# Kernel tuning notes

Measured on AMD Instinct MI355X. Metric: run time of the kernel, lower is better.

The kernel has to match this reference:

```python
import jax, jax.numpy as jnp
import numpy as np

K = 1.0      # Lorentz curvature param (geoopt convention: <x,x>_L = -K)
SQK = 1.0    # sqrt(K)
B, LOOKBACK, SEG, D = 256, 4096, 32, 256
N = LOOKBACK // SEG  # 128 segments


def _mink_inner(x, y):
    # Minkowski inner product, keepdims on last axis
    return -x[..., :1] * y[..., :1] + jnp.sum(x[..., 1:] * y[..., 1:], axis=-1, keepdims=True)


def _expmap0_spatial(v):
    # v: [..., D] spatial tangent at origin -> point on hyperboloid [..., D+1]
    n = jnp.linalg.norm(v, axis=-1, keepdims=True)
    ns = jnp.maximum(n, 1e-9)
    x0 = SQK * jnp.cosh(n / SQK)
    xr = SQK * jnp.sinh(n / SQK) * v / ns
    return jnp.concatenate([x0, xr], axis=-1)


def _projx(x):
    # re-project onto hyperboloid: x0 = sqrt(K + ||x_spatial||^2)
    xr = x[..., 1:]
    x0 = jnp.sqrt(K + jnp.sum(xr * xr, axis=-1, keepdims=True))
    return jnp.concatenate([x0, xr], axis=-1)


def _origin_like(x):
    return jnp.zeros_like(x).at[..., 0].set(SQK)


def _logmap(x, y):
    # log_x(y) on the Lorentz manifold
    alpha = jnp.maximum(-_mink_inner(x, y) / K, 1.0 + 1e-7)
    dist = SQK * jnp.arccosh(alpha)
    u = y - alpha * x  # tangent direction (unnormalized)
    un = jnp.sqrt(jnp.maximum(_mink_inner(u, u), 1e-12))
    return dist * u / un


def _expmap(x, u):
    # exp_x(u) on the Lorentz manifold
    un = jnp.sqrt(jnp.maximum(_mink_inner(u, u), 1e-12))
    theta = un / SQK
    return jnp.cosh(theta) * x + jnp.sinh(theta) * SQK * u / un


def _clip_norm(v, max_norm):
    # euclidean-norm clip (torch.norm semantics in source)
    n = jnp.linalg.norm(v, axis=-1, keepdims=True)
    return v / jnp.maximum(n, 1e-12) * jnp.minimum(n, max_norm)


def _encode(x, W, b):
    # [B, lookback] -> [B, N, D]; dropout is identity at eval
    xs = x.reshape(B, N, SEG)
    return jnp.einsum('bns,ds->bnd', xs, W) + b


def _to_hyperbolic(z, effective_scale):
    # vectorized over all segments (original looped over seg_idx)
    v = z * jnp.tanh(effective_scale)
    n = jnp.maximum(jnp.linalg.norm(v, axis=-1, keepdims=True), 1e-8)
    v = v / n * jnp.minimum(n, 1.5)
    return _projx(_expmap0_spatial(v))


def _lorentz_fusion(pts, w):
    # pts: [4, B, N, D+1], w: [4] softmax weights; weighted Karcher mean
    o = _origin_like(pts[0])
    t0 = _logmap(o, pts)                       # tangents at origin (time comp == 0)
    wt = _clip_norm(jnp.einsum('c,cbnd->bnd', w, t0), 2.0)
    mean = _projx(_expmap0_spatial(wt[..., 1:]))  # geoopt expmap0 uses spatial part
    for _ in range(5):                         # fixed 5 Karcher iterations
        tv = _logmap(mean, pts)                # [4, B, N, D+1]
        wv = _clip_norm(jnp.einsum('c,cbnd->bnd', w, tv), 2.0)
        mean = _projx(_expmap(mean, 0.1 * wv))
    return mean


def setup_inputs() -> dict:
    key = jax.random.key(0)
    ks = jax.random.split(key, 12)
    wscale = 1.0 / np.sqrt(SEG)
    inp = {
        'trend': jax.random.normal(ks[0], (B, LOOKBACK), jnp.float32),
        'seasonal_coarse': jax.random.normal(ks[1], (B, LOOKBACK), jnp.float32),
        'seasonal_fine': jax.random.normal(ks[2], (B, LOOKBACK), jnp.float32),
        'residual': jax.random.normal(ks[3], (B, LOOKBACK), jnp.float32),
        'W_trend': jax.random.normal(ks[4], (D, SEG), jnp.float32) * wscale,
        'b_trend': jnp.zeros((D,), jnp.float32),
        'W_coarse': jax.random.normal(ks[5], (D, SEG), jnp.float32) * wscale,
        'b_coarse': jnp.zeros((D,), jnp.float32),
        'W_fine': jax.random.normal(ks[6], (D, SEG), jnp.float32) * wscale,
        'b_fine': jnp.zeros((D,), jnp.float32),
        'W_residual': jax.random.normal(ks[7], (D, SEG), jnp.float32) * wscale,
        'b_residual': jnp.zeros((D,), jnp.float32),
        'effective_scale': jnp.asarray(0.001, jnp.float32),
        'lorentz_weights': jnp.ones((4,), jnp.float32) * 0.25,
    }
    return inp


def reference(trend, seasonal_coarse, seasonal_fine, residual,
              W_trend, b_trend, W_coarse, b_coarse, W_fine, b_fine,
              W_residual, b_residual, effective_scale, lorentz_weights):
    z_t = _encode(trend, W_trend, b_trend)
    z_c = _encode(seasonal_coarse, W_coarse, b_coarse)
    z_f = _encode(seasonal_fine, W_fine, b_fine)
    z_r = _encode(residual, W_residual, b_residual)
    h_t = _to_hyperbolic(z_t, effective_scale)
    h_c = _to_hyperbolic(z_c, effective_scale)
    h_f = _to_hyperbolic(z_f, effective_scale)
    h_r = _to_hyperbolic(z_r, effective_scale)
    w = jax.nn.softmax(lorentz_weights)
    combined = _lorentz_fusion(jnp.stack([h_t, h_c, h_f, h_r], axis=0), w)
    return (h_t, h_c, h_f, h_r, combined)
```

## Files before the change

kernel.cpp:

```cpp
#include <hip/hip_runtime.h>
#include <math.h>

namespace {

typedef float f4 __attribute__((ext_vector_type(4)));

constexpr int PPW  = 4;
constexpr int WPB  = 4;
constexpr int PPB  = PPW * WPB;
constexpr int NPTS = 256 * 128;
constexpr int GRID = NPTS / PPB;
constexpr int OUTS = 257;
constexpr size_t HOFF = (size_t)NPTS * OUTS;
constexpr int WSTR = 256;
constexpr int HSTR = 260;

__device__ __forceinline__ float frcp(float x)   { return __builtin_amdgcn_rcpf(x); }
__device__ __forceinline__ float fsqrt_(float x) { return __builtin_amdgcn_sqrtf(x); }
__device__ __forceinline__ float facosh(float a) {
  return __logf(a + fsqrt_(fmaf(a, a, -1.f)));
}
__device__ __forceinline__ void fsinhcosh(float x, float& sh, float& ch) {
  float e = __expf(x), ei = frcp(e);
  sh = 0.5f * (e - ei);
  ch = 0.5f * (e + ei);
}
__device__ __forceinline__ float fsinh(float x) {
  float e = __expf(x);
  return 0.5f * (e - frcp(e));
}
__device__ __forceinline__ float dot4(f4 a, f4 b) {
  return a.x * b.x + a.y * b.y + a.z * b.z + a.w * b.w;
}
__device__ __forceinline__ f4 fma4s(float a, f4 b, f4 c) {
  f4 av = {a, a, a, a};
  return __builtin_elementwise_fma(av, b, c);
}

template <int CTRL>
__device__ __forceinline__ float dpp_add(float x) {
  int t = __builtin_amdgcn_update_dpp(0, __builtin_bit_cast(int, x), CTRL, 0xf, 0xf, true);
  return x + __builtin_bit_cast(float, t);
}

template <int NB>
__device__ __forceinline__ void grp_reduce(float* v) {
#pragma unroll
  for (int i = 0; i < NB; ++i) {
    float t = v[i];
    t = dpp_add<0x128>(t);
    t = dpp_add<0x124>(t);
    t = dpp_add<0x122>(t);
    t = dpp_add<0x121>(t);
    v[i] = t;
  }
}

__global__ __launch_bounds__(256) void splmw_kernel(
    const float* __restrict__ xt, const float* __restrict__ xc,
    const float* __restrict__ xf, const float* __restrict__ xr,
    const float* __restrict__ Wt, const float* __restrict__ bt,
    const float* __restrict__ Wc, const float* __restrict__ bc,
    const float* __restrict__ Wf, const float* __restrict__ bf,
    const float* __restrict__ Wr, const float* __restrict__ br,
    const float* __restrict__ esp, const float* __restrict__ lwp,
    float* __restrict__ out) {
  __shared__ float wlds[32 * WSTR];
  __shared__ float hlds[WPB * PPW * HSTR];

  const int tid  = threadIdx.x;
  const int lane = tid & 63;
  const int m    = lane & 15;
  const int grp  = lane >> 4;
  const int wv   = __builtin_amdgcn_readfirstlane(tid >> 6);
  const int pt0  = blockIdx.x * PPB + wv * PPW;
  const int pt   = pt0 + grp;
  float* hw = hlds + wv * (PPW * HSTR);

  float es2 = __expf(2.f * esp[0]);
  const float ts = (es2 - 1.f) * frcp(es2 + 1.f);
  float l0 = lwp[0], l1 = lwp[1], l2 = lwp[2], l3 = lwp[3];
  float mx = fmaxf(fmaxf(l0, l1), fmaxf(l2, l3));
  float e0 = __expf(l0 - mx), e1 = __expf(l1 - mx);
  float e2 = __expf(l2 - mx), e3 = __expf(l3 - mx);
  float ei = frcp(e0 + e1 + e2 + e3);
  const float wgt[4] = {e0 * ei, e1 * ei, e2 * ei, e3 * ei};

  const float* xsarr[4] = {xt, xc, xf, xr};
  const float* Wsarr[4] = {Wt, Wc, Wf, Wr};
  const float* Bsarr[4] = {bt, bc, bf, br};

  f4    h[4][4];
  float x0s[4];
  float r2s[4];

#pragma unroll
  for (int c = 0; c < 4; ++c) {
    const float* Wp = Wsarr[c];
    f4 wrow[8];
#pragma unroll
    for (int k = 0; k < 8; ++k) wrow[k] = *(const f4*)(Wp + tid * 32 + 4 * k);
    __syncthreads();
#pragma unroll
    for (int k = 0; k < 8; ++k) {
      wlds[(4 * k + 0) * WSTR + tid] = wrow[k].x;
      wlds[(4 * k + 1) * WSTR + tid] = wrow[k].y;
      wlds[(4 * k + 2) * WSTR + tid] = wrow[k].z;
      wlds[(4 * k + 3) * WSTR + tid] = wrow[k].w;
    }
    __syncthreads();

    f4 acc[PPW];
    {
      f4 bv = ((const f4*)Bsarr[c])[lane];
#pragma unroll
      for (int p = 0; p < PPW; ++p) acc[p] = bv;
    }
    const float* xp = xsarr[c] + (size_t)pt0 * 32;
#pragma unroll
    for (int s4 = 0; s4 < 8; ++s4) {
      f4 q0 = *(const f4*)(xp + 4 * s4);
      f4 q1 = *(const f4*)(xp + 32 + 4 * s4);
      f4 q2 = *(const f4*)(xp + 64 + 4 * s4);
      f4 q3 = *(const f4*)(xp + 96 + 4 * s4);
      float qa[4][4] = {{q0.x, q0.y, q0.z, q0.w}, {q1.x, q1.y, q1.z, q1.w},
                        {q2.x, q2.y, q2.z, q2.w}, {q3.x, q3.y, q3.z, q3.w}};
#pragma unroll
      for (int si = 0; si < 4; ++si) {
        f4 w4 = *(const f4*)&wlds[(4 * s4 + si) * WSTR + 4 * lane];
#pragma unroll
        for (int p = 0; p < PPW; ++p) acc[p] = fma4s(qa[p][si], w4, acc[p]);
      }
    }

#pragma unroll
    for (int p = 0; p < PPW; ++p) *(f4*)&hw[p * HSTR + 4 * lane] = acc[p];
    __builtin_amdgcn_wave_barrier();
    f4 zj[4];
#pragma unroll
    for (int j = 0; j < 4; ++j) zj[j] = *(const f4*)&hw[grp * HSTR + 4 * m + 64 * j];

    float pa = 0.f;
#pragma unroll
    for (int j = 0; j < 4; ++j) {
      h[c][j] = ts * zj[j];
      pa += dot4(h[c][j], h[c][j]);
    }
    grp_reduce<1>(&pa);
    {
      float n1  = fsqrt_(pa);
      float n1m = fmaxf(n1, 1e-8f);
      float c1  = fminf(n1m, 1.5f) * frcp(n1m);
      float n2  = c1 * n1;
      float nsx = fmaxf(n2, 1e-9f);
      float sh  = fsinh(n2);
      float rn  = frcp(nsx);
      float g   = sh * c1 * rn;
      float sxr = sh * n2 * rn;
      float xx0 = fsqrt_(fmaf(sxr, sxr, 1.f));
#pragma unroll
      for (int j = 0; j < 4; ++j) h[c][j] = g * h[c][j];
      x0s[c] = xx0;
      r2s[c] = g * g * pa;
      float* o = out + (size_t)c * HOFF + (size_t)pt * OUTS;
      if (m == 0) o[0] = xx0;
#pragma unroll
      for (int j = 0; j < 4; ++j) {
        int base = 1 + 4 * m + 64 * j;
        f4 v = h[c][j];
        o[base] = v.x; o[base + 1] = v.y; o[base + 2] = v.z; o[base + 3] = v.w;
      }
    }
  }

  float wt0 = 0.f;
  f4    wtr[4];
#pragma unroll
  for (int j = 0; j < 4; ++j) wtr[j] = (f4){0.f, 0.f, 0.f, 0.f};
#pragma unroll
  for (int c = 0; c < 4; ++c) {
    float y0    = x0s[c];
    float alpha = fmaxf(y0, 1.f + 1e-7f);
    float dist  = facosh(alpha);
    float u0    = y0 - alpha;
    float msq   = r2s[c] - u0 * u0;
    float un    = fsqrt_(fmaxf(msq, 1e-12f));
    float f     = wgt[c] * dist * frcp(un);
    wt0 = fmaf(f, u0, wt0);
#pragma unroll
    for (int j = 0; j < 4; ++j) wtr[j] = fma4s(f, h[c][j], wtr[j]);
  }
  float rrp = 0.f;
#pragma unroll
  for (int j = 0; j < 4; ++j) rrp += dot4(wtr[j], wtr[j]);
  grp_reduce<1>(&rrp);

  f4    mr[4];
  float mrr, m0;
  {
    float rr  = rrp;
    float nrm = fsqrt_(fmaf(wt0, wt0, rr));
    float scl = fminf(nrm, 2.f) * frcp(fmaxf(nrm, 1e-12f));
    float nr  = scl * fsqrt_(rr);
    float nsx = fmaxf(nr, 1e-9f);
    float g   = fsinh(nr) * scl * frcp(nsx);
#pragma unroll
    for (int j = 0; j < 4; ++j) mr[j] = g * wtr[j];
    mrr = g * g * rr;
    m0  = fsqrt_(1.f + mrr);
  }

#pragma unroll 1
  for (int it = 0; it < 5; ++it) {
    float dots[4];
#pragma unroll
    for (int c = 0; c < 4; ++c) {
      float d = 0.f;
#pragma unroll
      for (int j = 0; j < 4; ++j) d += dot4(mr[j], h[c][j]);
      dots[c] = d;
    }
    grp_reduce<4>(dots);

    float wv0 = 0.f;
    f4    wvr[4];
#pragma unroll
    for (int j = 0; j < 4; ++j) wvr[j] = (f4){0.f, 0.f, 0.f, 0.f};
#pragma unroll
    for (int c = 0; c < 4; ++c) {
      float d     = dots[c];
      float y0    = x0s[c];
      float ip    = fmaf(m0, y0, -d);
      float alpha = fmaxf(ip, 1.f + 1e-7f);
      float dist  = facosh(alpha);
      float u0    = fmaf(-alpha, m0, y0);
      float t   = fmaf(alpha, mrr, -2.f * d);
      float s2  = fmaf(alpha, t, r2s[c]);
      float msq = s2 - u0 * u0;
      float un  = fsqrt_(fmaxf(msq, 1e-12f));
      float f   = wgt[c] * dist * frcp(un);
      wv0 = fmaf(f, u0, wv0);
#pragma unroll
      for (int j = 0; j < 4; ++j) {
        f4 diff = fma4s(-alpha, mr[j], h[c][j]);
        wvr[j]  = fma4s(f, diff, wvr[j]);
      }
    }
    float pr[2] = {0.f, 0.f};
#pragma unroll
    for (int j = 0; j < 4; ++j) {
      pr[0] += dot4(wvr[j], wvr[j]);
      pr[1] += dot4(mr[j], wvr[j]);
    }
    grp_reduce<2>(pr);

    {
      float rr2  = pr[0];
      float mwv  = pr[1];
      float nrm2 = fsqrt_(fmaf(wv0, wv0, rr2));
      float sc2  = fminf(nrm2, 2.f) * frcp(fmaxf(nrm2, 1e-12f));
      float tt   = 0.1f * sc2;
      float msqu = tt * tt * (rr2 - wv0 * wv0);
      float un2  = fsqrt_(fmaxf(msqu, 1e-12f));
      float shv, chv;
      fsinhcosh(un2, shv, chv);
      float gg = shv * tt * frcp(un2);
#pragma unroll
      for (int j = 0; j < 4; ++j) mr[j] = fma4s(chv, mr[j], gg * wvr[j]);
      mrr = chv * chv * mrr + 2.f * chv * gg * mwv + gg * gg * rr2;
      m0  = fsqrt_(1.f + mrr);
    }
  }

  {
    float* o = out + 4 * HOFF + (size_t)pt * OUTS;
    if (m == 0) o[0] = m0;
#pragma unroll
    for (int j = 0; j < 4; ++j) {
      int base = 1 + 4 * m + 64 * j;
      f4 v = mr[j];
      o[base] = v.x; o[base + 1] = v.y; o[base + 2] = v.z; o[base + 3] = v.w;
    }
  }
}

}

extern "C" void kernel_launch(void* const* d_in, const int* in_sizes, int n_in,
                              void* d_out, int out_size, void* d_ws, size_t ws_size,
                              hipStream_t stream) {
  (void)in_sizes; (void)n_in; (void)out_size; (void)d_ws; (void)ws_size;
  splmw_kernel<<<GRID, 256, 0, stream>>>(
      (const float*)d_in[0], (const float*)d_in[1], (const float*)d_in[2],
      (const float*)d_in[3], (const float*)d_in[4], (const float*)d_in[5],
      (const float*)d_in[6], (const float*)d_in[7], (const float*)d_in[8],
      (const float*)d_in[9], (const float*)d_in[10], (const float*)d_in[11],
      (const float*)d_in[12], (const float*)d_in[13], (float*)d_out);
}
```

Measured before the change: 268.8 us.

## Pre-transpose weights in a separate kernel and read them from global memory

Adds a small kernel that transposes the four encoder weight matrices into workspace once per call. The main kernel then loads the transposed weights straight from global memory (L2-cached) instead of staging them into LDS with two block-wide barriers per component. This removes the per-block LDS fill and __syncthreads stalls and frees 32 KB of LDS, which may allow more blocks to be resident. In exchange it adds a second launch and repeated global/L2 weight loads in the inner loop. An opaque zero offset is also added to the input pointer, apparently to steer code generation.

```diff
diff --git a/kernel.cpp b/kernel.cpp
--- a/kernel.cpp
+++ b/kernel.cpp
@@ -4,15 +4,15 @@
 namespace {
 
 typedef float f4 __attribute__((ext_vector_type(4)));
+
+constexpr int NPTS = 256 * 128;
+constexpr int OUTS = 257;
+constexpr size_t HOFF = (size_t)NPTS * OUTS;
 
 constexpr int PPW  = 4;
 constexpr int WPB  = 4;
 constexpr int PPB  = PPW * WPB;
-constexpr int NPTS = 256 * 128;
 constexpr int GRID = NPTS / PPB;
-constexpr int OUTS = 257;
-constexpr size_t HOFF = (size_t)NPTS * OUTS;
-constexpr int WSTR = 256;
 constexpr int HSTR = 260;
 
 __device__ __forceinline__ float frcp(float x)   { return __builtin_amdgcn_rcpf(x); }
@@ -56,16 +56,34 @@
   }
 }
 
-__global__ __launch_bounds__(256) void splmw_kernel(
+__global__ __launch_bounds__(256) void transpose_kernel(
+    const float* __restrict__ Wt, const float* __restrict__ Wc,
+    const float* __restrict__ Wf, const float* __restrict__ Wr,
+    float* __restrict__ wsT) {
+  const float* Wsarr[4] = {Wt, Wc, Wf, Wr};
+  const int c = blockIdx.x;
+  const int d = threadIdx.x;
+  const float* Wp = Wsarr[c];
+  f4 wrow[8];
+#pragma unroll
+  for (int k = 0; k < 8; ++k) wrow[k] = *(const f4*)(Wp + d * 32 + 4 * k);
+  float* o = wsT + c * 8192;
+#pragma unroll
+  for (int k = 0; k < 8; ++k) {
+    o[(4 * k + 0) * 256 + d] = wrow[k].x;
+    o[(4 * k + 1) * 256 + d] = wrow[k].y;
+    o[(4 * k + 2) * 256 + d] = wrow[k].z;
+    o[(4 * k + 3) * 256 + d] = wrow[k].w;
+  }
+}
+
+__global__ __launch_bounds__(256) void fused_kernel(
     const float* __restrict__ xt, const float* __restrict__ xc,
     const float* __restrict__ xf, const float* __restrict__ xr,
-    const float* __restrict__ Wt, const float* __restrict__ bt,
-    const float* __restrict__ Wc, const float* __restrict__ bc,
-    const float* __restrict__ Wf, const float* __restrict__ bf,
-    const float* __restrict__ Wr, const float* __restrict__ br,
+    const float* __restrict__ bt, const float* __restrict__ bc,
+    const float* __restrict__ bf, const float* __restrict__ br,
     const float* __restrict__ esp, const float* __restrict__ lwp,
-    float* __restrict__ out) {
-  __shared__ float wlds[32 * WSTR];
+    const float* __restrict__ wsT, float* __restrict__ out) {
   __shared__ float hlds[WPB * PPW * HSTR];
 
   const int tid  = threadIdx.x;
@@ -87,8 +105,10 @@
   const float wgt[4] = {e0 * ei, e1 * ei, e2 * ei, e3 * ei};
 
   const float* xsarr[4] = {xt, xc, xf, xr};
-  const float* Wsarr[4] = {Wt, Wc, Wf, Wr};
   const float* Bsarr[4] = {bt, bc, bf, br};
+
+  int lz = 0;
+  asm volatile("" : "+v"(lz));
 
   f4    h[4][4];
   float x0s[4];
@@ -96,40 +116,27 @@
 
 #pragma unroll
   for (int c = 0; c < 4; ++c) {
-    const float* Wp = Wsarr[c];
-    f4 wrow[8];
-#pragma unroll
-    for (int k = 0; k < 8; ++k) wrow[k] = *(const f4*)(Wp + tid * 32 + 4 * k);
-    __syncthreads();
-#pragma unroll
-    for (int k = 0; k < 8; ++k) {
-      wlds[(4 * k + 0) * WSTR + tid] = wrow[k].x;
-      wlds[(4 * k + 1) * WSTR + tid] = wrow[k].y;
-      wlds[(4 * k + 2) * WSTR + tid] = wrow[k].z;
-      wlds[(4 * k + 3) * WSTR + tid] = wrow[k].w;
-    }
-    __syncthreads();
-
     f4 acc[PPW];
     {
       f4 bv = ((const f4*)Bsarr[c])[lane];
 #pragma unroll
       for (int p = 0; p < PPW; ++p) acc[p] = bv;
     }
-    const float* xp = xsarr[c] + (size_t)pt0 * 32;
+    const float* xp = xsarr[c] + (size_t)pt0 * 32 + lz;
+    const float* wT = wsT + c * 8192 + 4 * lane;
 #pragma unroll
     for (int s4 = 0; s4 < 8; ++s4) {
-      f4 q0 = *(const f4*)(xp + 4 * s4);
-      f4 q1 = *(const f4*)(xp + 32 + 4 * s4);
-      f4 q2 = *(const f4*)(xp + 64 + 4 * s4);
-      f4 q3 = *(const f4*)(xp + 96 + 4 * s4);
-      float qa[4][4] = {{q0.x, q0.y, q0.z, q0.w}, {q1.x, q1.y, q1.z, q1.w},
-                        {q2.x, q2.y, q2.z, q2.w}, {q3.x, q3.y, q3.z, q3.w}};
-#pragma unroll
-      for (int si = 0; si < 4; ++si) {
-        f4 w4 = *(const f4*)&wlds[(4 * s4 + si) * WSTR + 4 * lane];
-#pragma unroll
-        for (int p = 0; p < PPW; ++p) acc[p] = fma4s(qa[p][si], w4, acc[p]);
+      f4 w4[4];
+#pragma unroll
+      for (int si = 0; si < 4; ++si)
+        w4[si] = *(const f4*)(wT + (4 * s4 + si) * 256);
+#pragma unroll
+      for (int p = 0; p < PPW; ++p) {
+        f4 xq = *(const f4*)(xp + 32 * p + 4 * s4);
+        acc[p] = fma4s(xq.x, w4[0], acc[p]);
+        acc[p] = fma4s(xq.y, w4[1], acc[p]);
+        acc[p] = fma4s(xq.z, w4[2], acc[p]);
+        acc[p] = fma4s(xq.w, w4[3], acc[p]);
       }
     }
 
@@ -139,6 +146,7 @@
     f4 zj[4];
 #pragma unroll
     for (int j = 0; j < 4; ++j) zj[j] = *(const f4*)&hw[grp * HSTR + 4 * m + 64 * j];
+    __builtin_amdgcn_wave_barrier();
 
     float pa = 0.f;
 #pragma unroll
@@ -289,11 +297,15 @@
 extern "C" void kernel_launch(void* const* d_in, const int* in_sizes, int n_in,
                               void* d_out, int out_size, void* d_ws, size_t ws_size,
                               hipStream_t stream) {
-  (void)in_sizes; (void)n_in; (void)out_size; (void)d_ws; (void)ws_size;
-  splmw_kernel<<<GRID, 256, 0, stream>>>(
+  (void)in_sizes; (void)n_in; (void)out_size; (void)ws_size;
+  float* out = (float*)d_out;
+  float* wsT = (float*)d_ws;
+  transpose_kernel<<<4, 256, 0, stream>>>(
+      (const float*)d_in[4], (const float*)d_in[6], (const float*)d_in[8],
+      (const float*)d_in[10], wsT);
+  fused_kernel<<<GRID, 256, 0, stream>>>(
       (const float*)d_in[0], (const float*)d_in[1], (const float*)d_in[2],
-      (const float*)d_in[3], (const float*)d_in[4], (const float*)d_in[5],
-      (const float*)d_in[6], (const float*)d_in[7], (const float*)d_in[8],
-      (const float*)d_in[9], (const float*)d_in[10], (const float*)d_in[11],
-      (const float*)d_in[12], (const float*)d_in[13], (float*)d_out);
-}
+      (const float*)d_in[3], (const float*)d_in[5], (const float*)d_in[7],
+      (const float*)d_in[9], (const float*)d_in[11], (const float*)d_in[12],
+      (const float*)d_in[13], wsT, out);
+}
```

Result: slower. 280.3 us (+4.3%).
